# Kernel optimization log

Hardware: AMD Instinct MI355X
Metric: run time of the kernel (lower is better)

Reference implementation:

```python
import jax, jax.numpy as jnp
import numpy as np

B, K, D = 16, 2048, 512
INNER = 2 * D  # expand * d_model
KW = 5        # d_conv=4 bumped to odd 5
EPS = 1e-5


def setup_inputs() -> dict:
    key = jax.random.key(0)
    ks = jax.random.split(key, 8)
    x = jax.random.normal(ks[0], (B, K, D), dtype=jnp.float32)
    norm_w = jnp.ones((D,), dtype=jnp.float32)
    Wa = jax.random.normal(ks[1], (INNER, D), dtype=jnp.float32) * (1.0 / np.sqrt(D))
    Wb = jax.random.normal(ks[2], (INNER, D), dtype=jnp.float32) * (1.0 / np.sqrt(D))
    conv_w = jax.random.normal(ks[3], (INNER, 1, KW), dtype=jnp.float32) * (1.0 / np.sqrt(KW))
    conv_b = jax.random.normal(ks[4], (INNER,), dtype=jnp.float32) * 0.01
    alpha = jnp.zeros((INNER,), dtype=jnp.float32)
    beta = jnp.ones((INNER,), dtype=jnp.float32)
    gamma = jnp.ones((INNER,), dtype=jnp.float32)
    delta = jnp.zeros((INNER,), dtype=jnp.float32)
    Wout = jax.random.normal(ks[5], (D, INNER), dtype=jnp.float32) * (1.0 / np.sqrt(INNER))
    return {"x": x, "norm_w": norm_w, "Wa": Wa, "Wb": Wb, "conv_w": conv_w,
            "conv_b": conv_b, "alpha": alpha, "beta": beta, "gamma": gamma,
            "delta": delta, "Wout": Wout}


def _rmsnorm(x, w):
    var = jnp.mean(x * x, axis=-1, keepdims=True)
    return x * jax.lax.rsqrt(var + EPS) * w


def _dwconv(a, conv_w, conv_b):
    # a: [B, INNER, K]; depthwise conv, 'same' padding (pad = KW//2)
    y = jax.lax.conv_general_dilated(
        a, conv_w,
        window_strides=(1,), padding=[(KW // 2, KW // 2)],
        dimension_numbers=("NCH", "OIH", "NCH"),
        feature_group_count=INNER)
    return y + conv_b[None, :, None]


def _selective_scan(u, alpha, beta, gamma, delta):
    # u: [B, K, INNER]; per-channel LTI recurrence s_t = a*s_{t-1} + b*u_t, y_t = g*s_t + d*u_t
    a = jax.nn.sigmoid(alpha)

    def step(s, ut):
        s = a * s + beta * ut
        return s, gamma * s + delta * ut

    u_t = jnp.transpose(u, (1, 0, 2))  # [K, B, INNER]
    s0 = jnp.zeros((u.shape[0], u.shape[2]), dtype=u.dtype)
    _, ys = jax.lax.scan(step, s0, u_t)
    return jnp.transpose(ys, (1, 0, 2))  # [B, K, INNER]


def reference(x, norm_w, Wa, Wb, conv_w, conv_b, alpha, beta, gamma, delta, Wout):
    h = _rmsnorm(x, norm_w)
    a = jnp.einsum("bkd,id->bki", h, Wa)  # [B,K,INNER]
    b = jnp.einsum("bkd,id->bki", h, Wb)
    a = jnp.transpose(a, (0, 2, 1))       # [B,INNER,K]
    a = _dwconv(a, conv_w, conv_b)
    a = jnp.transpose(a, (0, 2, 1))       # [B,K,INNER]
    a = jax.nn.silu(a)
    s = _selective_scan(a, alpha, beta, gamma, delta)
    g = s * b
    y = jnp.einsum("bki,di->bkd", g, Wout)
    return x + y
```

## Files before the change

kernel.cpp:

```cpp
#include <hip/hip_runtime.h>
#include <stdint.h>

#define B_ 16
#define K_ 2048
#define D_ 512
#define INNER_ 1024
#define M_ (B_*K_)
#define KW_ 5
#define EPS_ 1e-5f
#define NC_ 64
#define CL_ (K_/NC_)

typedef __attribute__((ext_vector_type(8))) short short8;
typedef __attribute__((ext_vector_type(4))) float f32x4;
typedef __attribute__((ext_vector_type(8))) float f32x8;

typedef const __attribute__((address_space(1))) unsigned int* gas_u32;
typedef __attribute__((address_space(3))) unsigned int* las_u32;

static __device__ __forceinline__ float bf2f(unsigned short u) {
    unsigned int v = ((unsigned int)u) << 16;
    return __builtin_bit_cast(float, v);
}
static __device__ __forceinline__ unsigned short f2bf(float f) {
    unsigned int x = __builtin_bit_cast(unsigned int, f);
    unsigned int r = (x + 0x7FFFu + ((x >> 16) & 1u)) >> 16;
    return (unsigned short)r;
}
static __device__ __forceinline__ f32x8 cvt8(short8 v) {
    f32x8 f;
    #pragma unroll
    for (int j = 0; j < 8; ++j) f[j] = bf2f((unsigned short)v[j]);
    return f;
}

__global__ __launch_bounds__(256) void k_wconv(const float* __restrict__ Wa,
                                               const float* __restrict__ Wb,
                                               const float* __restrict__ Wout,
                                               unsigned short* __restrict__ Wcat,
                                               unsigned short* __restrict__ WoutB) {
    const int NW = INNER_ * D_;
    int idx = blockIdx.x * 256 + threadIdx.x;
    if (idx < NW)            Wcat[idx]       = f2bf(Wa[idx]);
    else if (idx < 2 * NW)   Wcat[idx]       = f2bf(Wb[idx - NW]);
    else                     WoutB[idx-2*NW] = f2bf(Wout[idx - 2*NW]);
}

__global__ __launch_bounds__(256) void k_rmsnorm(const float* __restrict__ x,
                                                 const float* __restrict__ w,
                                                 unsigned short* __restrict__ h) {
    int row  = blockIdx.x * 4 + (threadIdx.x >> 6);
    int lane = threadIdx.x & 63;
    const float4* xr = (const float4*)(x + (size_t)row * D_);
    float4 v0 = xr[lane];
    float4 v1 = xr[64 + lane];
    float ss = v0.x*v0.x + v0.y*v0.y + v0.z*v0.z + v0.w*v0.w
             + v1.x*v1.x + v1.y*v1.y + v1.z*v1.z + v1.w*v1.w;
    #pragma unroll
    for (int off = 32; off; off >>= 1) ss += __shfl_xor(ss, off, 64);
    float r = rsqrtf(ss * (1.0f / D_) + EPS_);
    const float4* wv = (const float4*)w;
    float4 w0 = wv[lane], w1 = wv[64 + lane];
    ushort4 o0, o1;
    o0.x = f2bf(v0.x * r * w0.x); o0.y = f2bf(v0.y * r * w0.y);
    o0.z = f2bf(v0.z * r * w0.z); o0.w = f2bf(v0.w * r * w0.w);
    o1.x = f2bf(v1.x * r * w1.x); o1.y = f2bf(v1.y * r * w1.y);
    o1.z = f2bf(v1.z * r * w1.z); o1.w = f2bf(v1.w * r * w1.w);
    ushort4* hr = (ushort4*)(h + (size_t)row * D_);
    hr[lane]      = o0;
    hr[64 + lane] = o1;
}

template<int EPI>
__global__ __launch_bounds__(256) void k_gemm_bt(
    const unsigned short* __restrict__ A,
    const unsigned short* __restrict__ Bw,
    void* __restrict__ Cv,
    const float* __restrict__ Xadd,
    int Kd, int Nld)
{
    __shared__ __align__(16) unsigned short lA[128 * 64];
    __shared__ __align__(16) unsigned short lB[128 * 64];
    const int tid  = threadIdx.x;
    const int w    = tid >> 6, lane = tid & 63;
    const int wr   = w >> 1,   wc   = w & 1;
    const int m0   = blockIdx.x * 128, n0 = blockIdx.y * 128;

    const int srow = tid >> 3;
    const int scol = ((tid & 7) ^ (srow & 7)) << 3;

    f32x4 acc[4][4];
    #pragma unroll
    for (int i = 0; i < 4; ++i)
        #pragma unroll
        for (int j = 0; j < 4; ++j) acc[i][j] = (f32x4){0.f, 0.f, 0.f, 0.f};

    const int lrow = lane & 15;
    const int kb16 = (lane >> 4) << 4;

    for (int kt = 0; kt < Kd; kt += 64) {
        #pragma unroll
        for (int j = 0; j < 4; ++j) {
            const unsigned short* gA = A + (size_t)(m0 + j*32 + srow) * Kd + kt + scol;
            __builtin_amdgcn_global_load_lds((gas_u32)gA, (las_u32)(lA + j*2048 + w*512), 16, 0, 0);
            const unsigned short* gB = Bw + (size_t)(n0 + j*32 + srow) * Kd + kt + scol;
            __builtin_amdgcn_global_load_lds((gas_u32)gB, (las_u32)(lB + j*2048 + w*512), 16, 0, 0);
        }
        __syncthreads();
        #pragma unroll
        for (int kk = 0; kk < 2; ++kk) {
            short8 af[4], bfr[4];
            #pragma unroll
            for (int i = 0; i < 4; ++i) {
                int rowa  = wr*64 + i*16 + lrow;
                int addra = rowa*128 + ((kk*64 + kb16) ^ ((rowa & 7) << 4));
                af[i]  = *(const short8*)((const char*)lA + addra);
                int rowb  = wc*64 + i*16 + lrow;
                int addrb = rowb*128 + ((kk*64 + kb16) ^ ((rowb & 7) << 4));
                bfr[i] = *(const short8*)((const char*)lB + addrb);
            }
            #pragma unroll
            for (int i = 0; i < 4; ++i)
                #pragma unroll
                for (int j = 0; j < 4; ++j)
                    acc[i][j] = __builtin_amdgcn_mfma_f32_16x16x32_bf16(af[i], bfr[j], acc[i][j], 0, 0, 0);
        }
        __syncthreads();
    }

    #pragma unroll
    for (int i = 0; i < 4; ++i) {
        int mrow = m0 + wr*64 + i*16 + ((lane >> 4) << 2);
        #pragma unroll
        for (int j = 0; j < 4; ++j) {
            int ncol = n0 + wc*64 + j*16 + (lane & 15);
            f32x4 v = acc[i][j];
            #pragma unroll
            for (int r = 0; r < 4; ++r) {
                size_t off = (size_t)(mrow + r) * Nld + ncol;
                if (EPI == 0) ((unsigned short*)Cv)[off] = f2bf(v[r]);
                else          ((float*)Cv)[off] = Xadd[off] + v[r];
            }
        }
    }
}

__global__ __launch_bounds__(256) void k_prefix(const float* __restrict__ alpha,
                                                const float* __restrict__ sEnd,
                                                float* __restrict__ sPre) {
    int idx = blockIdx.x * 256 + threadIdx.x;
    int b = idx >> 10, i = idx & 1023;
    float Aa = 1.f / (1.f + __expf(-alpha[i]));
    float Ap = Aa;
    #pragma unroll
    for (int t = 0; t < 5; ++t) Ap = Ap * Ap;
    float s = 0.f;
    for (int c = 0; c < NC_; ++c) {
        size_t off = ((size_t)(b * NC_ + c)) * INNER_ + i;
        sPre[off] = s;
        s = s * Ap + sEnd[off];
    }
}

template<int PASS>
__global__ __launch_bounds__(256) void k_scan(
    const unsigned short* __restrict__ ab,
    const float* __restrict__ conv_w, const float* __restrict__ conv_b,
    const float* __restrict__ alpha,  const float* __restrict__ beta,
    const float* __restrict__ gamma,  const float* __restrict__ delta,
    float* __restrict__ sEnd, const float* __restrict__ sPre,
    unsigned short* __restrict__ g)
{
    const int tid = threadIdx.x;
    const int c   = blockIdx.x * 2 + (tid >> 7);
    const int b   = blockIdx.y;
    const int ch  = (tid & 127) * 8;

    f32x8 w0, w1, w2, w3, w4, bias, Aa, bet, gam, del;
    #pragma unroll
    for (int j = 0; j < 8; ++j) {
        int i = ch + j;
        w0[j] = conv_w[i*KW_+0]; w1[j] = conv_w[i*KW_+1]; w2[j] = conv_w[i*KW_+2];
        w3[j] = conv_w[i*KW_+3]; w4[j] = conv_w[i*KW_+4];
        bias[j] = conv_b[i];
        Aa[j]  = 1.f / (1.f + __expf(-alpha[i]));
        bet[j] = beta[i];
        if (PASS == 1) { gam[j] = gamma[i]; del[j] = delta[i]; }
    }

    const int k0 = c * CL_;
    const size_t rowbase = (size_t)b * K_;

    #define LDV(k) (((unsigned)(k) < (unsigned)K_) \
        ? cvt8(*(const short8*)(ab + (rowbase + (k)) * 2048 + ch)) \
        : (f32x8){0.f,0.f,0.f,0.f,0.f,0.f,0.f,0.f})

    f32x8 am2 = LDV(k0 - 2), am1 = LDV(k0 - 1), a0v = LDV(k0), ap1 = LDV(k0 + 1);

    f32x8 s;
    if (PASS == 1) {
        s = *(const f32x8*)(sPre + ((size_t)(b * NC_ + c)) * INNER_ + ch);
    } else {
        #pragma unroll
        for (int j = 0; j < 8; ++j) s[j] = 0.f;
    }

    #pragma unroll 2
    for (int kk = 0; kk < CL_; ++kk) {
        int k = k0 + kk;
        f32x8 ap2 = LDV(k + 2);
        f32x8 v = w0*am2 + w1*am1 + w2*a0v + w3*ap1 + w4*ap2 + bias;
        f32x8 u;
        #pragma unroll
        for (int j = 0; j < 8; ++j) u[j] = v[j] / (1.f + __expf(-v[j]));
        s = Aa * s + bet * u;
        if (PASS == 1) {
            f32x8 bv = cvt8(*(const short8*)(ab + (rowbase + k) * 2048 + INNER_ + ch));
            f32x8 gv = (gam * s + del * u) * bv;
            short8 o;
            #pragma unroll
            for (int j = 0; j < 8; ++j) o[j] = (short)f2bf(gv[j]);
            *(short8*)(g + (rowbase + k) * INNER_ + ch) = o;
        }
        am2 = am1; am1 = a0v; a0v = ap1; ap1 = ap2;
    }
    if (PASS == 0)
        *(f32x8*)(sEnd + ((size_t)(b * NC_ + c)) * INNER_ + ch) = s;
    #undef LDV
}

extern "C" void kernel_launch(void* const* d_in, const int* in_sizes, int n_in,
                              void* d_out, int out_size, void* d_ws, size_t ws_size,
                              hipStream_t stream) {
    const float* x      = (const float*)d_in[0];
    const float* norm_w = (const float*)d_in[1];
    const float* Wa     = (const float*)d_in[2];
    const float* Wb     = (const float*)d_in[3];
    const float* conv_w = (const float*)d_in[4];
    const float* conv_b = (const float*)d_in[5];
    const float* alpha  = (const float*)d_in[6];
    const float* beta   = (const float*)d_in[7];
    const float* gamma  = (const float*)d_in[8];
    const float* delta  = (const float*)d_in[9];
    const float* Wout   = (const float*)d_in[10];
    float* out = (float*)d_out;

    char* ws = (char*)d_ws;
    unsigned short* h    = (unsigned short*)ws; ws += (size_t)M_ * D_ * 2;
    unsigned short* Wcat = (unsigned short*)ws; ws += (size_t)2048 * 512 * 2;
    unsigned short* WoB  = (unsigned short*)ws; ws += (size_t)512 * 1024 * 2;
    unsigned short* abb  = (unsigned short*)ws; ws += (size_t)M_ * 2048 * 2;
    unsigned short* g    = (unsigned short*)ws; ws += (size_t)M_ * 1024 * 2;
    float* sEnd          = (float*)ws;          ws += (size_t)B_ * NC_ * INNER_ * 4;
    float* sPre          = (float*)ws;          ws += (size_t)B_ * NC_ * INNER_ * 4;

    k_wconv  <<<6144, 256, 0, stream>>>(Wa, Wb, Wout, Wcat, WoB);
    k_rmsnorm<<<M_ / 4, 256, 0, stream>>>(x, norm_w, h);
    k_gemm_bt<0><<<dim3(M_ / 128, 2048 / 128), 256, 0, stream>>>(h, Wcat, abb, nullptr, 512, 2048);
    k_scan<0><<<dim3(NC_ / 2, B_), 256, 0, stream>>>(abb, conv_w, conv_b, alpha, beta, gamma, delta, sEnd, nullptr, g);
    k_prefix<<<64, 256, 0, stream>>>(alpha, sEnd, sPre);
    k_scan<1><<<dim3(NC_ / 2, B_), 256, 0, stream>>>(abb, conv_w, conv_b, alpha, beta, gamma, delta, sEnd, sPre, g);
    k_gemm_bt<1><<<dim3(M_ / 128, 512 / 128), 256, 0, stream>>>(g, WoB, out, x, 1024, 512);
}
```

Before: 389.8 us.

## Replace GEMM with 256x256 double-buffered tile kernel with block swizzle

```diff
diff --git a/kernel.cpp b/kernel.cpp
--- a/kernel.cpp
+++ b/kernel.cpp
@@ -72,69 +72,108 @@
 }
 
 template<int EPI>
-__global__ __launch_bounds__(256) void k_gemm_bt(
+__global__ __launch_bounds__(512) void k_gemm256(
     const unsigned short* __restrict__ A,
     const unsigned short* __restrict__ Bw,
     void* __restrict__ Cv,
     const float* __restrict__ Xadd,
     int Kd, int Nld)
 {
-    __shared__ __align__(16) unsigned short lA[128 * 64];
-    __shared__ __align__(16) unsigned short lB[128 * 64];
+    __shared__ __align__(16) unsigned short lA[2][256 * 64];
+    __shared__ __align__(16) unsigned short lB[2][256 * 64];
     const int tid  = threadIdx.x;
     const int w    = tid >> 6, lane = tid & 63;
-    const int wr   = w >> 1,   wc   = w & 1;
-    const int m0   = blockIdx.x * 128, n0 = blockIdx.y * 128;
-
-    const int srow = tid >> 3;
-    const int scol = ((tid & 7) ^ (srow & 7)) << 3;
-
-    f32x4 acc[4][4];
-    #pragma unroll
-    for (int i = 0; i < 4; ++i)
-        #pragma unroll
-        for (int j = 0; j < 4; ++j) acc[i][j] = (f32x4){0.f, 0.f, 0.f, 0.f};
+    const int wr   = w >> 2,   wc   = w & 3;
+
+    const int nwg = gridDim.x * gridDim.y;
+    const int fid = blockIdx.y * gridDim.x + blockIdx.x;
+    const int swz = (fid & 7) * (nwg >> 3) + (fid >> 3);
+    const int m0  = (swz % gridDim.x) * 256;
+    const int n0  = (swz / gridDim.x) * 256;
+
+    const int srow = w * 8 + (lane >> 3);
+    const int scol = ((lane & 7) ^ (lane >> 3)) << 3;
+    const int NT   = Kd >> 6;
+
+    auto stage = [&](int t, int buf) {
+        const int kt = t << 6;
+        const unsigned short* ga = A  + (size_t)(m0 + srow) * Kd + kt + scol;
+        const unsigned short* gb = Bw + (size_t)(n0 + srow) * Kd + kt + scol;
+        #pragma unroll
+        for (int j = 0; j < 4; ++j) {
+            __builtin_amdgcn_global_load_lds((gas_u32)(ga + (size_t)j * 64 * Kd),
+                                             (las_u32)(&lA[buf][(j * 64 + w * 8) * 64]), 16, 0, 0);
+            __builtin_amdgcn_global_load_lds((gas_u32)(gb + (size_t)j * 64 * Kd),
+                                             (las_u32)(&lB[buf][(j * 64 + w * 8) * 64]), 16, 0, 0);
+        }
+    };
+
+    f32x4 acc[8][4];
+    #pragma unroll
+    for (int m = 0; m < 8; ++m)
+        #pragma unroll
+        for (int n = 0; n < 4; ++n) acc[m][n] = (f32x4){0.f, 0.f, 0.f, 0.f};
 
     const int lrow = lane & 15;
-    const int kb16 = (lane >> 4) << 4;
-
-    for (int kt = 0; kt < Kd; kt += 64) {
-        #pragma unroll
-        for (int j = 0; j < 4; ++j) {
-            const unsigned short* gA = A + (size_t)(m0 + j*32 + srow) * Kd + kt + scol;
-            __builtin_amdgcn_global_load_lds((gas_u32)gA, (las_u32)(lA + j*2048 + w*512), 16, 0, 0);
-            const unsigned short* gB = Bw + (size_t)(n0 + j*32 + srow) * Kd + kt + scol;
-            __builtin_amdgcn_global_load_lds((gas_u32)gB, (las_u32)(lB + j*2048 + w*512), 16, 0, 0);
-        }
-        __syncthreads();
-        #pragma unroll
-        for (int kk = 0; kk < 2; ++kk) {
-            short8 af[4], bfr[4];
+    const int hb   = (lane >> 4) << 4;
+    const int xr   = (lrow & 7) << 4;
+
+    stage(0, 0);
+    stage(1, 1);
+
+    for (int t = 0; t < NT; ++t) {
+        const int buf = t & 1;
+        if (t + 1 < NT) asm volatile("s_waitcnt vmcnt(8)" ::: "memory");
+        else            asm volatile("s_waitcnt vmcnt(0)" ::: "memory");
+        __builtin_amdgcn_s_barrier();
+
+        const char* pa = (const char*)lA[buf];
+        const char* pb = (const char*)lB[buf];
+
+        short8 a0[8], b0[4];
+        #pragma unroll
+        for (int m = 0; m < 8; ++m)
+            a0[m] = *(const short8*)(pa + (wr*128 + m*16 + lrow) * 128 + (hb ^ xr));
+        #pragma unroll
+        for (int n = 0; n < 4; ++n)
+            b0[n] = *(const short8*)(pb + (wc*64 + n*16 + lrow) * 128 + (hb ^ xr));
+
+        __builtin_amdgcn_s_setprio(1);
+        #pragma unroll
+        for (int m = 0; m < 8; ++m)
             #pragma unroll
-            for (int i = 0; i < 4; ++i) {
-                int rowa  = wr*64 + i*16 + lrow;
-                int addra = rowa*128 + ((kk*64 + kb16) ^ ((rowa & 7) << 4));
-                af[i]  = *(const short8*)((const char*)lA + addra);
-                int rowb  = wc*64 + i*16 + lrow;
-                int addrb = rowb*128 + ((kk*64 + kb16) ^ ((rowb & 7) << 4));
-                bfr[i] = *(const short8*)((const char*)lB + addrb);
-            }
+            for (int n = 0; n < 4; ++n)
+                acc[m][n] = __builtin_amdgcn_mfma_f32_16x16x32_bf16(a0[m], b0[n], acc[m][n], 0, 0, 0);
+        __builtin_amdgcn_s_setprio(0);
+
+        short8 a1[8], b1[4];
+        #pragma unroll
+        for (int m = 0; m < 8; ++m)
+            a1[m] = *(const short8*)(pa + (wr*128 + m*16 + lrow) * 128 + ((64 + hb) ^ xr));
+        #pragma unroll
+        for (int n = 0; n < 4; ++n)
+            b1[n] = *(const short8*)(pb + (wc*64 + n*16 + lrow) * 128 + ((64 + hb) ^ xr));
+
+        asm volatile("s_waitcnt lgkmcnt(0)" ::: "memory");
+        __builtin_amdgcn_s_barrier();
+        if (t + 2 < NT) stage(t + 2, buf);
+
+        __builtin_amdgcn_s_setprio(1);
+        #pragma unroll
+        for (int m = 0; m < 8; ++m)
             #pragma unroll
-            for (int i = 0; i < 4; ++i)
-                #pragma unroll
-                for (int j = 0; j < 4; ++j)
-                    acc[i][j] = __builtin_amdgcn_mfma_f32_16x16x32_bf16(af[i], bfr[j], acc[i][j], 0, 0, 0);
-        }
-        __syncthreads();
-    }
-
-    #pragma unroll
-    for (int i = 0; i < 4; ++i) {
-        int mrow = m0 + wr*64 + i*16 + ((lane >> 4) << 2);
-        #pragma unroll
-        for (int j = 0; j < 4; ++j) {
-            int ncol = n0 + wc*64 + j*16 + (lane & 15);
-            f32x4 v = acc[i][j];
+            for (int n = 0; n < 4; ++n)
+                acc[m][n] = __builtin_amdgcn_mfma_f32_16x16x32_bf16(a1[m], b1[n], acc[m][n], 0, 0, 0);
+        __builtin_amdgcn_s_setprio(0);
+    }
+
+    #pragma unroll
+    for (int m = 0; m < 8; ++m) {
+        int mrow = m0 + wr*128 + m*16 + ((lane >> 4) << 2);
+        #pragma unroll
+        for (int n = 0; n < 4; ++n) {
+            int ncol = n0 + wc*64 + n*16 + (lane & 15);
+            f32x4 v = acc[m][n];
             #pragma unroll
             for (int r = 0; r < 4; ++r) {
                 size_t off = (size_t)(mrow + r) * Nld + ncol;
@@ -256,9 +295,9 @@
 
     k_wconv  <<<6144, 256, 0, stream>>>(Wa, Wb, Wout, Wcat, WoB);
     k_rmsnorm<<<M_ / 4, 256, 0, stream>>>(x, norm_w, h);
-    k_gemm_bt<0><<<dim3(M_ / 128, 2048 / 128), 256, 0, stream>>>(h, Wcat, abb, nullptr, 512, 2048);
+    k_gemm256<0><<<dim3(M_ / 256, 2048 / 256), 512, 0, stream>>>(h, Wcat, abb, nullptr, 512, 2048);
     k_scan<0><<<dim3(NC_ / 2, B_), 256, 0, stream>>>(abb, conv_w, conv_b, alpha, beta, gamma, delta, sEnd, nullptr, g);
     k_prefix<<<64, 256, 0, stream>>>(alpha, sEnd, sPre);
     k_scan<1><<<dim3(NC_ / 2, B_), 256, 0, stream>>>(abb, conv_w, conv_b, alpha, beta, gamma, delta, sEnd, sPre, g);
-    k_gemm_bt<1><<<dim3(M_ / 128, 512 / 128), 256, 0, stream>>>(g, WoB, out, x, 1024, 512);
-}
+    k_gemm256<1><<<dim3(M_ / 256, 512 / 256), 512, 0, stream>>>(g, WoB, out, x, 1024, 512);
+}
```

After: 366.3 us. 1.06x faster.
